# Kernel tuning notes

Hardware: AMD Instinct MI355X
Metric: run time of the kernel (lower is better)

The kernel has to match this reference:

```python
import jax, jax.numpy as jnp
import numpy as np

NEG_SLOPE = 0.2


def gat_conv(x, src, dst, W, a_src, a_dst, bias, heads, out_ch, concat, num_nodes):
    # x: [N, F_in]; W: [F_in, heads*out_ch]
    h = (x @ W).reshape(num_nodes, heads, out_ch)          # [N, H, C]
    alpha_s = jnp.sum(h * a_src, axis=-1)                   # [N, H]
    alpha_d = jnp.sum(h * a_dst, axis=-1)                   # [N, H]
    e = jax.nn.leaky_relu(alpha_s[src] + alpha_d[dst], NEG_SLOPE)  # [E, H]
    # segment softmax over destination node (numerically stable)
    m = jax.ops.segment_max(e, dst, num_segments=num_nodes)        # [N, H]
    e = jnp.exp(e - m[dst])
    denom = jax.ops.segment_sum(e, dst, num_segments=num_nodes)    # [N, H]
    alpha = e / (denom[dst] + 1e-16)                               # [E, H]
    msg = h[src] * alpha[:, :, None]                               # [E, H, C]
    out = jax.ops.segment_sum(msg, dst, num_segments=num_nodes)    # [N, H, C]
    if concat:
        out = out.reshape(num_nodes, heads * out_ch)
    else:
        out = out.mean(axis=1)
    return out + bias


def setup_inputs() -> dict:
    key = jax.random.key(0)
    ks = jax.random.split(key, 12)
    N, E, F_in, H, C = 50000, 800000, 30, 4, 128
    s = lambda fan: 1.0 / np.sqrt(fan)
    inp = {
        "x": jax.random.normal(ks[0], (N, F_in), jnp.float32),
        "edge_index": jax.random.randint(ks[1], (2, E), 0, N, jnp.int32),
        "W1": jax.random.normal(ks[2], (F_in, H * C), jnp.float32) * s(F_in),
        "a1_src": jax.random.normal(ks[3], (H, C), jnp.float32) * s(C),
        "a1_dst": jax.random.normal(ks[4], (H, C), jnp.float32) * s(C),
        "b1": jnp.zeros((H * C,), jnp.float32),
        "W2": jax.random.normal(ks[5], (H * C, H * C), jnp.float32) * s(H * C),
        "a2_src": jax.random.normal(ks[6], (H, C), jnp.float32) * s(C),
        "a2_dst": jax.random.normal(ks[7], (H, C), jnp.float32) * s(C),
        "b2": jnp.zeros((H * C,), jnp.float32),
        "W3": jax.random.normal(ks[8], (H * C, H * 1), jnp.float32) * s(H * C),
        "a3_src": jax.random.normal(ks[9], (H, 1), jnp.float32),
        "a3_dst": jax.random.normal(ks[10], (H, 1), jnp.float32),
        "b3": jnp.zeros((1,), jnp.float32),
    }
    return inp


def reference(x, edge_index, W1, a1_src, a1_dst, b1, W2, a2_src, a2_dst, b2,
              W3, a3_src, a3_dst, b3):
    N = x.shape[0]
    # PyG GATConv adds self loops by default
    loop = jnp.arange(N, dtype=edge_index.dtype)
    src = jnp.concatenate([edge_index[0], loop])
    dst = jnp.concatenate([edge_index[1], loop])

    h = gat_conv(x, src, dst, W1, a1_src, a1_dst, b1, 4, 128, True, N)
    h = jax.nn.relu(h)  # dropout is a no-op in eval mode
    h = gat_conv(h, src, dst, W2, a2_src, a2_dst, b2, 4, 128, True, N)
    h = jax.nn.relu(h)
    out = gat_conv(h, src, dst, W3, a3_src, a3_dst, b3, 4, 1, False, N)
    return out  # [N, 1]
```

## Files before the change

kernel.cpp:

```cpp
#include <hip/hip_runtime.h>

#define NEG_SLOPE 0.2f

constexpr int F = 512;
constexpr int F_IN = 30;

typedef short bfrag __attribute__((ext_vector_type(8)));
typedef float f32x4 __attribute__((ext_vector_type(4)));

__device__ __forceinline__ unsigned short bf16_rne(float v) {
  unsigned u = __float_as_uint(v);
  u += 0x7FFF + ((u >> 16) & 1);
  return (unsigned short)(u >> 16);
}
__device__ __forceinline__ float bf16f(unsigned short h) {
  return __uint_as_float(((unsigned)h) << 16);
}


__global__ void hist_kernel(const int* __restrict__ ei, int* __restrict__ counts,
                            int N, int E) {
  int e = blockIdx.x * blockDim.x + threadIdx.x;
  int Et = E + N;
  if (e >= Et) return;
  int d = (e < E) ? ei[E + e] : (e - E);
  atomicAdd(&counts[d], 1);
}

__global__ void scan_kernel(const int* __restrict__ counts, int* __restrict__ offsets,
                            int* __restrict__ cursor, int n) {
  __shared__ int wsum[16];
  __shared__ int carry_s;
  int tid = threadIdx.x;
  int lane = tid & 63, wid = tid >> 6;
  if (tid == 0) carry_s = 0;
  __syncthreads();
  for (int base = 0; base < n; base += 1024) {
    int i = base + tid;
    int v = (i < n) ? counts[i] : 0;
    int x = v;
#pragma unroll
    for (int d = 1; d < 64; d <<= 1) {
      int t2 = __shfl_up(x, d);
      if (lane >= d) x += t2;
    }
    if (lane == 63) wsum[wid] = x;
    __syncthreads();
    if (wid == 0) {
      int ws = (lane < 16) ? wsum[lane] : 0;
#pragma unroll
      for (int d = 1; d < 16; d <<= 1) {
        int t2 = __shfl_up(ws, d);
        if (lane >= d) ws += t2;
      }
      if (lane < 16) wsum[lane] = ws;
    }
    __syncthreads();
    int wpre = (wid > 0) ? wsum[wid - 1] : 0;
    int excl = carry_s + wpre + x - v;
    if (i < n) { offsets[i] = excl; cursor[i] = excl; }
    __syncthreads();
    if (tid == 0) carry_s += wsum[15];
    __syncthreads();
  }
  if (threadIdx.x == 0) offsets[n] = carry_s;
}

__global__ void scatter_kernel(const int* __restrict__ ei, int* __restrict__ cursor,
                               int* __restrict__ src_s, int N, int E) {
  int e = blockIdx.x * blockDim.x + threadIdx.x;
  int Et = E + N;
  if (e >= Et) return;
  int s, d;
  if (e < E) { s = ei[e]; d = ei[E + e]; } else { s = e - E; d = e - E; }
  int p = atomicAdd(&cursor[d], 1);
  src_s[p] = s;
}

__global__ void segsort_kernel(int* __restrict__ src_s, const int* __restrict__ off, int N) {
  int n = blockIdx.x * blockDim.x + threadIdx.x;
  if (n >= N) return;
  int p0 = off[n], p1 = off[n + 1];
  for (int i = p0 + 1; i < p1; ++i) {
    int key = src_s[i];
    int j = i - 1;
    while (j >= p0 && src_s[j] > key) { src_s[j + 1] = src_s[j]; --j; }
    src_s[j + 1] = key;
  }
}


__global__ void gemm30_kernel(const float* __restrict__ X, const float* __restrict__ W,
                              float* __restrict__ out, int N) {
  __shared__ float xs[16][F_IN];
  int row0 = blockIdx.x * 16;
  int tid = threadIdx.x;
  for (int i = tid; i < 16 * F_IN; i += 256) {
    int r = i / F_IN, k = i - r * F_IN;
    int row = row0 + r;
    xs[r][k] = (row < N) ? X[(size_t)row * F_IN + k] : 0.f;
  }
  __syncthreads();
  int cg = tid & 127;
  int rg = tid >> 7;
  int c0 = cg * 4;
  float4 acc[8];
#pragma unroll
  for (int r = 0; r < 8; ++r) acc[r] = make_float4(0.f, 0.f, 0.f, 0.f);
#pragma unroll 2
  for (int k = 0; k < F_IN; ++k) {
    float4 w = *(const float4*)(W + (size_t)k * F + c0);
#pragma unroll
    for (int r = 0; r < 8; ++r) {
      float xv = xs[rg * 8 + r][k];
      acc[r].x += xv * w.x; acc[r].y += xv * w.y;
      acc[r].z += xv * w.z; acc[r].w += xv * w.w;
    }
  }
#pragma unroll
  for (int r = 0; r < 8; ++r) {
    int row = row0 + rg * 8 + r;
    if (row < N) *(float4*)(out + (size_t)row * F + c0) = acc[r];
  }
}


__global__ void wsplit_kernel(const float* __restrict__ W,
                              unsigned short* __restrict__ Wth,
                              unsigned short* __restrict__ Wtl) {
  __shared__ float t[64][65];
  int bx = blockIdx.x & 7, by = blockIdx.x >> 3;
  int tid = threadIdx.x;
#pragma unroll
  for (int i = 0; i < 16; ++i) {
    int idx = tid + i * 256;
    int r = idx >> 6, c = idx & 63;
    t[r][c] = W[(size_t)(by * 64 + r) * 512 + bx * 64 + c];
  }
  __syncthreads();
#pragma unroll
  for (int i = 0; i < 16; ++i) {
    int idx = tid + i * 256;
    int r = idx >> 6, c = idx & 63;
    float v = t[c][r];
    unsigned short hi = bf16_rne(v);
    unsigned short lo = bf16_rne(v - bf16f(hi));
    size_t o = (size_t)(bx * 64 + r) * 512 + by * 64 + c;
    Wth[o] = hi; Wtl[o] = lo;
  }
}


__global__ void gemm512_mfma(const unsigned short* __restrict__ Xhi,
                             const unsigned short* __restrict__ Xlo,
                             const unsigned short* __restrict__ Wth,
                             const unsigned short* __restrict__ Wtl,
                             float* __restrict__ out, int N) {
  __shared__ int4 lds4[2048];
  char* lds = (char*)lds4;
  const int tid = threadIdx.x;
  const int wid = tid >> 6;
  const int lane = tid & 63;
  const int row0 = blockIdx.x * 128;
  const int col0 = blockIdx.y * 128;
  const int wr = wid >> 1, wc = wid & 1;

  const unsigned short* sb = (wid == 0) ? Xhi : (wid == 1) ? Xlo : (wid == 2) ? Wth : Wtl;
  const int tile0 = (wid < 2) ? row0 : col0;
  const int chunk = (lane & 3) ^ ((lane >> 3) & 3);
  const unsigned short* lanesrc = sb + (size_t)(tile0 + (lane >> 2)) * 512 + chunk * 8;
  char* ldst = lds + wid * 8192;

  const int g = lane >> 4;
  int aoff[4], boff[4];
#pragma unroll
  for (int m = 0; m < 4; ++m) {
    int r = wr * 64 + m * 16 + (lane & 15);
    aoff[m] = r * 64 + ((g ^ ((r >> 1) & 3)) << 4);
    int c = wc * 64 + m * 16 + (lane & 15);
    boff[m] = c * 64 + ((g ^ ((c >> 1) & 3)) << 4);
  }

  f32x4 acc[4][4];
#pragma unroll
  for (int m = 0; m < 4; ++m)
#pragma unroll
    for (int n = 0; n < 4; ++n) acc[m][n] = f32x4{0.f, 0.f, 0.f, 0.f};

  for (int kc = 0; kc < 16; ++kc) {
#pragma unroll
    for (int i = 0; i < 8; ++i) {
      __builtin_amdgcn_global_load_lds(
          (const __attribute__((address_space(1))) void*)(lanesrc + i * 8192 + kc * 32),
          (__attribute__((address_space(3))) void*)(ldst + i * 1024), 16, 0, 0);
    }
    __syncthreads();
    bfrag ah[4], al[4], bh[4], bl[4];
#pragma unroll
    for (int m = 0; m < 4; ++m) {
      ah[m] = *(const bfrag*)(lds + aoff[m]);
      al[m] = *(const bfrag*)(lds + 8192 + aoff[m]);
      bh[m] = *(const bfrag*)(lds + 16384 + boff[m]);
      bl[m] = *(const bfrag*)(lds + 24576 + boff[m]);
    }
#pragma unroll
    for (int m = 0; m < 4; ++m)
#pragma unroll
      for (int n = 0; n < 4; ++n) {
        acc[m][n] = __builtin_amdgcn_mfma_f32_16x16x32_bf16(al[m], bh[n], acc[m][n], 0, 0, 0);
        acc[m][n] = __builtin_amdgcn_mfma_f32_16x16x32_bf16(ah[m], bl[n], acc[m][n], 0, 0, 0);
        acc[m][n] = __builtin_amdgcn_mfma_f32_16x16x32_bf16(ah[m], bh[n], acc[m][n], 0, 0, 0);
      }
    __syncthreads();
  }

  const int crow = (lane >> 4) * 4, ccol = lane & 15;
#pragma unroll
  for (int m = 0; m < 4; ++m) {
    int Rb = row0 + wr * 64 + m * 16 + crow;
#pragma unroll
    for (int n = 0; n < 4; ++n) {
      int C = col0 + wc * 64 + n * 16 + ccol;
#pragma unroll
      for (int q = 0; q < 4; ++q) {
        int R = Rb + q;
        if (R < N) out[(size_t)R * F + C] = acc[m][n][q];
      }
    }
  }
}

__global__ void gemm3_kernel(const float* __restrict__ X, const float* __restrict__ W3,
                             float* __restrict__ h3, int N) {
  int n = blockIdx.x * 4 + (threadIdx.x >> 6);
  int lane = threadIdx.x & 63;
  if (n >= N) return;
  float acc[4] = {0.f, 0.f, 0.f, 0.f};
  for (int k = lane; k < F; k += 64) {
    float xv = X[(size_t)n * F + k];
#pragma unroll
    for (int j = 0; j < 4; ++j) acc[j] += xv * W3[k * 4 + j];
  }
#pragma unroll
  for (int j = 0; j < 4; ++j)
    for (int off = 32; off > 0; off >>= 1) acc[j] += __shfl_down(acc[j], off);
  if (lane == 0) {
    float4 o; o.x = acc[0]; o.y = acc[1]; o.z = acc[2]; o.w = acc[3];
    *(float4*)(h3 + (size_t)n * 4) = o;
  }
}


__global__ void alpha_kernel(const float* __restrict__ h, const float* __restrict__ asrc,
                             const float* __restrict__ adst, float* __restrict__ as,
                             float* __restrict__ ad) {
  int n = blockIdx.x;
  int tid = threadIdx.x;
  int c0 = tid * 4;
  float4 hv = *(const float4*)(h + (size_t)n * F + c0);
  float4 sa = *(const float4*)(asrc + c0);
  float4 da = *(const float4*)(adst + c0);
  float ps = hv.x * sa.x + hv.y * sa.y + hv.z * sa.z + hv.w * sa.w;
  float pd = hv.x * da.x + hv.y * da.y + hv.z * da.z + hv.w * da.w;
#pragma unroll
  for (int off = 16; off > 0; off >>= 1) {
    ps += __shfl_down(ps, off);
    pd += __shfl_down(pd, off);
  }
  if ((tid & 31) == 0) {
    int head = tid >> 5;
    as[n * 4 + head] = ps;
    ad[n * 4 + head] = pd;
  }
}

__global__ void alpha3_kernel(const float* __restrict__ h3, const float* __restrict__ a3s,
                              const float* __restrict__ a3d, float* __restrict__ as,
                              float* __restrict__ ad, int N) {
  int t = blockIdx.x * blockDim.x + threadIdx.x;
  if (t >= N * 4) return;
  int hh = t & 3;
  float v = h3[t];
  as[t] = v * a3s[hh];
  ad[t] = v * a3d[hh];
}


__device__ __forceinline__ float leaky(float v) { return v > 0.f ? v : NEG_SLOPE * v; }

__device__ __forceinline__ void fma4(float4& a, float s, const float4& b) {
  a.x += s * b.x; a.y += s * b.y; a.z += s * b.z; a.w += s * b.w;
}

template <bool RELU, bool SPLIT>
__global__ void fused_aggregate_kernel(const float* __restrict__ hsrc,
                                       const float* __restrict__ as, const float* __restrict__ ad,
                                       const int* __restrict__ src_s, const int* __restrict__ off,
                                       const float* __restrict__ bias, float* __restrict__ out,
                                       unsigned short* __restrict__ oh, unsigned short* __restrict__ ol) {
  int n = blockIdx.x;
  int tid = threadIdx.x;
  int head = tid >> 5;
  int l32 = tid & 31;
  int c0 = tid * 4;
  int p0 = off[n], p1 = off[n + 1];
  float adv = ad[n * 4 + head];

  float m = -1e30f, s = 0.f;
  for (int p = p0 + l32; p < p1; p += 32) {
    float e = leaky(as[src_s[p] * 4 + head] + adv);
    if (e > m) { s *= __expf(m - e); m = e; }
    s += __expf(e - m);
  }
#pragma unroll
  for (int o = 16; o > 0; o >>= 1) {
    float mo = __shfl_down(m, o, 32);
    float so = __shfl_down(s, o, 32);
    float mn = fmaxf(m, mo);
    s = s * __expf(m - mn) + so * __expf(mo - mn);
    m = mn;
  }
  m = __shfl(m, 0, 32);
  s = __shfl(s, 0, 32);
  float inv = 1.f / (s + 1e-16f);

  float4 acc = make_float4(0.f, 0.f, 0.f, 0.f);
#pragma unroll 2
  for (int p = p0; p < p1; ++p) {
    int sp = src_s[p];
    float a = __expf(leaky(as[sp * 4 + head] + adv) - m) * inv;
    float4 hv = *(const float4*)(hsrc + (size_t)sp * F + c0);
    fma4(acc, a, hv);
  }
  float4 bv = *(const float4*)(bias + c0);
  acc.x += bv.x; acc.y += bv.y; acc.z += bv.z; acc.w += bv.w;
  if (RELU) {
    acc.x = fmaxf(acc.x, 0.f); acc.y = fmaxf(acc.y, 0.f);
    acc.z = fmaxf(acc.z, 0.f); acc.w = fmaxf(acc.w, 0.f);
  }
  if (SPLIT) {
    ushort4 hv4, lv4;
    hv4.x = bf16_rne(acc.x); lv4.x = bf16_rne(acc.x - bf16f(hv4.x));
    hv4.y = bf16_rne(acc.y); lv4.y = bf16_rne(acc.y - bf16f(hv4.y));
    hv4.z = bf16_rne(acc.z); lv4.z = bf16_rne(acc.z - bf16f(hv4.z));
    hv4.w = bf16_rne(acc.w); lv4.w = bf16_rne(acc.w - bf16f(hv4.w));
    *(ushort4*)(oh + (size_t)n * F + c0) = hv4;
    *(ushort4*)(ol + (size_t)n * F + c0) = lv4;
  } else {
    *(float4*)(out + (size_t)n * F + c0) = acc;
  }
}

__global__ void fused_aggregate3_kernel(const float* __restrict__ h3,
                                        const float* __restrict__ as, const float* __restrict__ ad,
                                        const int* __restrict__ src_s, const int* __restrict__ off,
                                        const float* __restrict__ b3, float* __restrict__ out, int N) {
  int t = blockIdx.x * blockDim.x + threadIdx.x;
  if (t >= N * 4) return;
  int n = t >> 2, head = t & 3;
  int p0 = off[n], p1 = off[n + 1];
  float adv = ad[t];
  float m = -1e30f, s = 0.f;
  for (int p = p0; p < p1; ++p) {
    float e = leaky(as[src_s[p] * 4 + head] + adv);
    if (e > m) { s *= __expf(m - e); m = e; }
    s += __expf(e - m);
  }
  float inv = 1.f / (s + 1e-16f);
  float acc = 0.f;
  for (int p = p0; p < p1; ++p) {
    int sp = src_s[p];
    float a = __expf(leaky(as[sp * 4 + head] + adv) - m) * inv;
    acc += a * h3[(size_t)sp * 4 + head];
  }
  acc += __shfl_down(acc, 1);
  acc += __shfl_down(acc, 2);
  if (head == 0) out[n] = acc * 0.25f + b3[0];
}


extern "C" void kernel_launch(void* const* d_in, const int* in_sizes, int n_in,
                              void* d_out, int out_size, void* d_ws, size_t ws_size,
                              hipStream_t stream) {
  const float* x   = (const float*)d_in[0];
  const int*   ei  = (const int*)d_in[1];
  const float* W1  = (const float*)d_in[2];
  const float* a1s = (const float*)d_in[3];
  const float* a1d = (const float*)d_in[4];
  const float* b1  = (const float*)d_in[5];
  const float* W2  = (const float*)d_in[6];
  const float* a2s = (const float*)d_in[7];
  const float* a2d = (const float*)d_in[8];
  const float* b2  = (const float*)d_in[9];
  const float* W3  = (const float*)d_in[10];
  const float* a3s = (const float*)d_in[11];
  const float* a3d = (const float*)d_in[12];
  const float* b3  = (const float*)d_in[13];

  const int N = in_sizes[0] / F_IN;
  const int E = in_sizes[1] / 2;
  const int Et = E + N;
  const int Npad = (N + 127) & ~127;

  char* base = (char*)d_ws;
  size_t off = 0;
  auto alloc = [&](size_t bytes) {
    void* p = base + off;
    off = (off + bytes + 255) & ~(size_t)255;
    return p;
  };
  float* A      = (float*)alloc((size_t)N * F * sizeof(float));
  float* U      = (float*)alloc((size_t)Npad * F * sizeof(float));
  unsigned short* Xhi = (unsigned short*)U;
  unsigned short* Xlo = Xhi + (size_t)Npad * F;
  float* Bbuf   = U;
  int*   src_s  = (int*)alloc((size_t)Et * sizeof(int));
  int*   counts = (int*)alloc((size_t)N * sizeof(int));
  int*   offs   = (int*)alloc((size_t)(N + 1) * sizeof(int));
  int*   cursor = (int*)alloc((size_t)N * sizeof(int));
  float* as     = (float*)alloc((size_t)N * 4 * sizeof(float));
  float* ad     = (float*)alloc((size_t)N * 4 * sizeof(float));
  float* h3     = (float*)alloc((size_t)N * 4 * sizeof(float));
  unsigned short* Wth = (unsigned short*)alloc((size_t)512 * 512 * sizeof(unsigned short));
  unsigned short* Wtl = (unsigned short*)alloc((size_t)512 * 512 * sizeof(unsigned short));

  hipMemsetAsync(counts, 0, (size_t)N * sizeof(int), stream);
  {
    int gg = (Et + 255) / 256;
    hipLaunchKernelGGL(hist_kernel, dim3(gg), dim3(256), 0, stream, ei, counts, N, E);
    hipLaunchKernelGGL(scan_kernel, dim3(1), dim3(1024), 0, stream, counts, offs, cursor, N);
    hipLaunchKernelGGL(scatter_kernel, dim3(gg), dim3(256), 0, stream, ei, cursor, src_s, N, E);
    hipLaunchKernelGGL(segsort_kernel, dim3((N + 255) / 256), dim3(256), 0, stream, src_s, offs, N);
    hipLaunchKernelGGL(wsplit_kernel, dim3(64), dim3(256), 0, stream, W2, Wth, Wtl);
  }

  int nhGrid = (N * 4 + 255) / 256;

  hipLaunchKernelGGL(gemm30_kernel, dim3((N + 15) / 16), dim3(256), 0, stream, x, W1, A, N);
  hipLaunchKernelGGL(alpha_kernel, dim3(N), dim3(128), 0, stream, A, a1s, a1d, as, ad);
  hipLaunchKernelGGL((fused_aggregate_kernel<true, true>), dim3(N), dim3(128), 0, stream,
                     A, as, ad, src_s, offs, b1, (float*)nullptr, Xhi, Xlo);

  hipLaunchKernelGGL(gemm512_mfma, dim3((N + 127) / 128, 4), dim3(256), 0, stream,
                     Xhi, Xlo, Wth, Wtl, A, N);
  hipLaunchKernelGGL(alpha_kernel, dim3(N), dim3(128), 0, stream, A, a2s, a2d, as, ad);
  hipLaunchKernelGGL((fused_aggregate_kernel<true, false>), dim3(N), dim3(128), 0, stream,
                     A, as, ad, src_s, offs, b2, Bbuf,
                     (unsigned short*)nullptr, (unsigned short*)nullptr);

  hipLaunchKernelGGL(gemm3_kernel, dim3((N + 3) / 4), dim3(256), 0, stream, Bbuf, W3, h3, N);
  hipLaunchKernelGGL(alpha3_kernel, dim3(nhGrid), dim3(256), 0, stream, h3, a3s, a3d, as, ad, N);
  hipLaunchKernelGGL(fused_aggregate3_kernel, dim3(nhGrid), dim3(256), 0, stream,
                     h3, as, ad, src_s, offs, b3, (float*)d_out, N);
}
```

Measured before the change: 990.7 us.

## Fuse attention coefficient computation into GEMM epilogues and parallelize offset scan

Computes the per-node source/destination attention scores directly in the epilogues of the three projection GEMMs, using shuffle and LDS reductions, and removes the standalone alpha kernels. This avoids re-reading the large projected feature matrices from memory. The single-block serial prefix scan over node degrees is replaced by a block-level scan, a block-sum scan and an add pass. The cost is extra epilogue work and register pressure in the GEMMs, plus two more small launches for the scan.

```diff
diff --git a/kernel.cpp b/kernel.cpp
--- a/kernel.cpp
+++ b/kernel.cpp
@@ -27,43 +27,74 @@
   atomicAdd(&counts[d], 1);
 }
 
-__global__ void scan_kernel(const int* __restrict__ counts, int* __restrict__ offsets,
-                            int* __restrict__ cursor, int n) {
+__global__ void blockscan_kernel(const int* __restrict__ counts, int* __restrict__ offsets,
+                                 int* __restrict__ bsums, int n) {
   __shared__ int wsum[16];
-  __shared__ int carry_s;
   int tid = threadIdx.x;
   int lane = tid & 63, wid = tid >> 6;
-  if (tid == 0) carry_s = 0;
-  __syncthreads();
-  for (int base = 0; base < n; base += 1024) {
-    int i = base + tid;
-    int v = (i < n) ? counts[i] : 0;
-    int x = v;
-#pragma unroll
-    for (int d = 1; d < 64; d <<= 1) {
-      int t2 = __shfl_up(x, d);
-      if (lane >= d) x += t2;
-    }
-    if (lane == 63) wsum[wid] = x;
-    __syncthreads();
-    if (wid == 0) {
-      int ws = (lane < 16) ? wsum[lane] : 0;
-#pragma unroll
-      for (int d = 1; d < 16; d <<= 1) {
-        int t2 = __shfl_up(ws, d);
-        if (lane >= d) ws += t2;
-      }
-      if (lane < 16) wsum[lane] = ws;
-    }
-    __syncthreads();
-    int wpre = (wid > 0) ? wsum[wid - 1] : 0;
-    int excl = carry_s + wpre + x - v;
-    if (i < n) { offsets[i] = excl; cursor[i] = excl; }
-    __syncthreads();
-    if (tid == 0) carry_s += wsum[15];
-    __syncthreads();
-  }
-  if (threadIdx.x == 0) offsets[n] = carry_s;
+  int i = blockIdx.x * 1024 + tid;
+  int v = (i < n) ? counts[i] : 0;
+  int x = v;
+#pragma unroll
+  for (int d = 1; d < 64; d <<= 1) {
+    int t2 = __shfl_up(x, d);
+    if (lane >= d) x += t2;
+  }
+  if (lane == 63) wsum[wid] = x;
+  __syncthreads();
+  if (wid == 0) {
+    int ws = (lane < 16) ? wsum[lane] : 0;
+#pragma unroll
+    for (int d = 1; d < 16; d <<= 1) {
+      int t2 = __shfl_up(ws, d);
+      if (lane >= d) ws += t2;
+    }
+    if (lane < 16) wsum[lane] = ws;
+  }
+  __syncthreads();
+  int excl = ((wid > 0) ? wsum[wid - 1] : 0) + x - v;
+  if (i < n) offsets[i] = excl;
+  if (tid == 0) bsums[blockIdx.x] = wsum[15];
+}
+
+__global__ void sumscan_kernel(const int* __restrict__ bsums, int* __restrict__ boffs, int nb) {
+  __shared__ int wsum[16];
+  int tid = threadIdx.x;
+  int lane = tid & 63, wid = tid >> 6;
+  int v = (tid < nb) ? bsums[tid] : 0;
+  int x = v;
+#pragma unroll
+  for (int d = 1; d < 64; d <<= 1) {
+    int t2 = __shfl_up(x, d);
+    if (lane >= d) x += t2;
+  }
+  if (lane == 63) wsum[wid] = x;
+  __syncthreads();
+  if (wid == 0) {
+    int ws = (lane < 16) ? wsum[lane] : 0;
+#pragma unroll
+    for (int d = 1; d < 16; d <<= 1) {
+      int t2 = __shfl_up(ws, d);
+      if (lane >= d) ws += t2;
+    }
+    if (lane < 16) wsum[lane] = ws;
+  }
+  __syncthreads();
+  int excl = ((wid > 0) ? wsum[wid - 1] : 0) + x - v;
+  if (tid <= nb) boffs[tid] = (tid < nb) ? excl : wsum[15];
+  if (tid == 0 && nb == 1024) boffs[1024] = wsum[15];
+}
+
+__global__ void scanadd_kernel(int* __restrict__ offsets, const int* __restrict__ boffs,
+                               int* __restrict__ cursor, int n, int nb) {
+  int i = blockIdx.x * blockDim.x + threadIdx.x;
+  if (i < n) {
+    int o = offsets[i] + boffs[i >> 10];
+    offsets[i] = o;
+    cursor[i] = o;
+  } else if (i == n) {
+    offsets[n] = boffs[nb];
+  }
 }
 
 __global__ void scatter_kernel(const int* __restrict__ ei, int* __restrict__ cursor,
@@ -91,7 +122,9 @@
 
 
 __global__ void gemm30_kernel(const float* __restrict__ X, const float* __restrict__ W,
-                              float* __restrict__ out, int N) {
+                              const float* __restrict__ a_s, const float* __restrict__ a_d,
+                              float* __restrict__ out,
+                              float* __restrict__ as_o, float* __restrict__ ad_o, int N) {
   __shared__ float xs[16][F_IN];
   int row0 = blockIdx.x * 16;
   int tid = threadIdx.x;
@@ -121,6 +154,23 @@
   for (int r = 0; r < 8; ++r) {
     int row = row0 + rg * 8 + r;
     if (row < N) *(float4*)(out + (size_t)row * F + c0) = acc[r];
+  }
+  int hd = cg >> 5;
+  float4 s4 = *(const float4*)(a_s + c0);
+  float4 d4 = *(const float4*)(a_d + c0);
+#pragma unroll
+  for (int r = 0; r < 8; ++r) {
+    float ps = acc[r].x * s4.x + acc[r].y * s4.y + acc[r].z * s4.z + acc[r].w * s4.w;
+    float pd = acc[r].x * d4.x + acc[r].y * d4.y + acc[r].z * d4.z + acc[r].w * d4.w;
+#pragma unroll
+    for (int o = 1; o < 32; o <<= 1) {
+      ps += __shfl_xor(ps, o, 32);
+      pd += __shfl_xor(pd, o, 32);
+    }
+    if ((tid & 31) == 0) {
+      int row = row0 + rg * 8 + r;
+      if (row < N) { as_o[row * 4 + hd] = ps; ad_o[row * 4 + hd] = pd; }
+    }
   }
 }
 
@@ -155,14 +205,17 @@
                              const unsigned short* __restrict__ Xlo,
                              const unsigned short* __restrict__ Wth,
                              const unsigned short* __restrict__ Wtl,
-                             float* __restrict__ out, int N) {
+                             const float* __restrict__ a_s, const float* __restrict__ a_d,
+                             float* __restrict__ out,
+                             float* __restrict__ as_o, float* __restrict__ ad_o, int N) {
   __shared__ int4 lds4[2048];
   char* lds = (char*)lds4;
   const int tid = threadIdx.x;
   const int wid = tid >> 6;
   const int lane = tid & 63;
   const int row0 = blockIdx.x * 128;
-  const int col0 = blockIdx.y * 128;
+  const int by = blockIdx.y;
+  const int col0 = by * 128;
   const int wr = wid >> 1, wc = wid & 1;
 
   const unsigned short* sb = (wid == 0) ? Xhi : (wid == 1) ? Xlo : (wid == 2) ? Wth : Wtl;
@@ -228,10 +281,50 @@
       }
     }
   }
+
+  float cs[4], cd[4];
+#pragma unroll
+  for (int n = 0; n < 4; ++n) {
+    cs[n] = a_s[col0 + wc * 64 + n * 16 + (lane & 15)];
+    cd[n] = a_d[col0 + wc * 64 + n * 16 + (lane & 15)];
+  }
+  float* red = (float*)lds;
+#pragma unroll
+  for (int m = 0; m < 4; ++m) {
+#pragma unroll
+    for (int q = 0; q < 4; ++q) {
+      float ps = 0.f, pd = 0.f;
+#pragma unroll
+      for (int n = 0; n < 4; ++n) {
+        ps += acc[m][n][q] * cs[n];
+        pd += acc[m][n][q] * cd[n];
+      }
+#pragma unroll
+      for (int o = 1; o < 16; o <<= 1) {
+        ps += __shfl_xor(ps, o, 16);
+        pd += __shfl_xor(pd, o, 16);
+      }
+      if ((lane & 15) == 0) {
+        int rl = m * 16 + (lane >> 4) * 4 + q;
+        red[((wr * 2 + wc) * 64 + rl) * 2 + 0] = ps;
+        red[((wr * 2 + wc) * 64 + rl) * 2 + 1] = pd;
+      }
+    }
+  }
+  __syncthreads();
+  if (tid < 128) {
+    int wrr = tid >> 6, rl = tid & 63;
+    float vs = red[((wrr * 2 + 0) * 64 + rl) * 2] + red[((wrr * 2 + 1) * 64 + rl) * 2];
+    float vd = red[((wrr * 2 + 0) * 64 + rl) * 2 + 1] + red[((wrr * 2 + 1) * 64 + rl) * 2 + 1];
+    int row = row0 + wrr * 64 + rl;
+    if (row < N) { as_o[row * 4 + by] = vs; ad_o[row * 4 + by] = vd; }
+  }
 }
 
 __global__ void gemm3_kernel(const float* __restrict__ X, const float* __restrict__ W3,
-                             float* __restrict__ h3, int N) {
+                             const float* __restrict__ a3s, const float* __restrict__ a3d,
+                             float* __restrict__ h3,
+                             float* __restrict__ as_o, float* __restrict__ ad_o, int N) {
   int n = blockIdx.x * 4 + (threadIdx.x >> 6);
   int lane = threadIdx.x & 63;
   if (n >= N) return;
@@ -247,42 +340,14 @@
   if (lane == 0) {
     float4 o; o.x = acc[0]; o.y = acc[1]; o.z = acc[2]; o.w = acc[3];
     *(float4*)(h3 + (size_t)n * 4) = o;
-  }
-}
-
-
-__global__ void alpha_kernel(const float* __restrict__ h, const float* __restrict__ asrc,
-                             const float* __restrict__ adst, float* __restrict__ as,
-                             float* __restrict__ ad) {
-  int n = blockIdx.x;
-  int tid = threadIdx.x;
-  int c0 = tid * 4;
-  float4 hv = *(const float4*)(h + (size_t)n * F + c0);
-  float4 sa = *(const float4*)(asrc + c0);
-  float4 da = *(const float4*)(adst + c0);
-  float ps = hv.x * sa.x + hv.y * sa.y + hv.z * sa.z + hv.w * sa.w;
-  float pd = hv.x * da.x + hv.y * da.y + hv.z * da.z + hv.w * da.w;
-#pragma unroll
-  for (int off = 16; off > 0; off >>= 1) {
-    ps += __shfl_down(ps, off);
-    pd += __shfl_down(pd, off);
-  }
-  if ((tid & 31) == 0) {
-    int head = tid >> 5;
-    as[n * 4 + head] = ps;
-    ad[n * 4 + head] = pd;
-  }
-}
-
-__global__ void alpha3_kernel(const float* __restrict__ h3, const float* __restrict__ a3s,
-                              const float* __restrict__ a3d, float* __restrict__ as,
-                              float* __restrict__ ad, int N) {
-  int t = blockIdx.x * blockDim.x + threadIdx.x;
-  if (t >= N * 4) return;
-  int hh = t & 3;
-  float v = h3[t];
-  as[t] = v * a3s[hh];
-  ad[t] = v * a3d[hh];
+    float4 so, dd;
+    so.x = acc[0] * a3s[0]; so.y = acc[1] * a3s[1];
+    so.z = acc[2] * a3s[2]; so.w = acc[3] * a3s[3];
+    dd.x = acc[0] * a3d[0]; dd.y = acc[1] * a3d[1];
+    dd.z = acc[2] * a3d[2]; dd.w = acc[3] * a3d[3];
+    *(float4*)(as_o + (size_t)n * 4) = so;
+    *(float4*)(ad_o + (size_t)n * 4) = dd;
+  }
 }
 
 
@@ -401,6 +466,7 @@
   const int E = in_sizes[1] / 2;
   const int Et = E + N;
   const int Npad = (N + 127) & ~127;
+  const int nb = (N + 1023) >> 10;
 
   char* base = (char*)d_ws;
   size_t off = 0;
@@ -418,6 +484,8 @@
   int*   counts = (int*)alloc((size_t)N * sizeof(int));
   int*   offs   = (int*)alloc((size_t)(N + 1) * sizeof(int));
   int*   cursor = (int*)alloc((size_t)N * sizeof(int));
+  int*   bsums  = (int*)alloc((size_t)1025 * sizeof(int));
+  int*   boffs  = (int*)alloc((size_t)1026 * sizeof(int));
   float* as     = (float*)alloc((size_t)N * 4 * sizeof(float));
   float* ad     = (float*)alloc((size_t)N * 4 * sizeof(float));
   float* h3     = (float*)alloc((size_t)N * 4 * sizeof(float));
@@ -428,7 +496,9 @@
   {
     int gg = (Et + 255) / 256;
     hipLaunchKernelGGL(hist_kernel, dim3(gg), dim3(256), 0, stream, ei, counts, N, E);
-    hipLaunchKernelGGL(scan_kernel, dim3(1), dim3(1024), 0, stream, counts, offs, cursor, N);
+    hipLaunchKernelGGL(blockscan_kernel, dim3(nb), dim3(1024), 0, stream, counts, offs, bsums, N);
+    hipLaunchKernelGGL(sumscan_kernel, dim3(1), dim3(1024), 0, stream, bsums, boffs, nb);
+    hipLaunchKernelGGL(scanadd_kernel, dim3((N + 256) / 256), dim3(256), 0, stream, offs, boffs, cursor, N, nb);
     hipLaunchKernelGGL(scatter_kernel, dim3(gg), dim3(256), 0, stream, ei, cursor, src_s, N, E);
     hipLaunchKernelGGL(segsort_kernel, dim3((N + 255) / 256), dim3(256), 0, stream, src_s, offs, N);
     hipLaunchKernelGGL(wsplit_kernel, dim3(64), dim3(256), 0, stream, W2, Wth, Wtl);
@@ -436,20 +506,19 @@
 
   int nhGrid = (N * 4 + 255) / 256;
 
-  hipLaunchKernelGGL(gemm30_kernel, dim3((N + 15) / 16), dim3(256), 0, stream, x, W1, A, N);
-  hipLaunchKernelGGL(alpha_kernel, dim3(N), dim3(128), 0, stream, A, a1s, a1d, as, ad);
+  hipLaunchKernelGGL(gemm30_kernel, dim3((N + 15) / 16), dim3(256), 0, stream,
+                     x, W1, a1s, a1d, A, as, ad, N);
   hipLaunchKernelGGL((fused_aggregate_kernel<true, true>), dim3(N), dim3(128), 0, stream,
                      A, as, ad, src_s, offs, b1, (float*)nullptr, Xhi, Xlo);
 
   hipLaunchKernelGGL(gemm512_mfma, dim3((N + 127) / 128, 4), dim3(256), 0, stream,
-                     Xhi, Xlo, Wth, Wtl, A, N);
-  hipLaunchKernelGGL(alpha_kernel, dim3(N), dim3(128), 0, stream, A, a2s, a2d, as, ad);
+                     Xhi, Xlo, Wth, Wtl, a2s, a2d, A, as, ad, N);
   hipLaunchKernelGGL((fused_aggregate_kernel<true, false>), dim3(N), dim3(128), 0, stream,
                      A, as, ad, src_s, offs, b2, Bbuf,
                      (unsigned short*)nullptr, (unsigned short*)nullptr);
 
-  hipLaunchKernelGGL(gemm3_kernel, dim3((N + 3) / 4), dim3(256), 0, stream, Bbuf, W3, h3, N);
-  hipLaunchKernelGGL(alpha3_kernel, dim3(nhGrid), dim3(256), 0, stream, h3, a3s, a3d, as, ad, N);
+  hipLaunchKernelGGL(gemm3_kernel, dim3((N + 3) / 4), dim3(256), 0, stream,
+                     Bbuf, W3, a3s, a3d, h3, as, ad, N);
   hipLaunchKernelGGL(fused_aggregate3_kernel, dim3(nhGrid), dim3(256), 0, stream,
                      h3, as, ad, src_s, offs, b3, (float*)d_out, N);
 }
```

Result: faster. 924.6 us (-6.7%).
